# Optimization experiments

Measured on AMD Instinct MI355X. Metric: run time of the kernel, lower is better.

Reference implementation:

```python
import jax, jax.numpy as jnp
import numpy as np

E, T, H, I, K = 32, 2048, 1024, 512, 4


def setup_inputs() -> dict:
    key = jax.random.key(0)
    k1, k2, k3, k4, k5 = jax.random.split(key, 5)
    hidden_states = jax.random.normal(k1, (T, H), dtype=jnp.float32)
    top_k_index = jax.random.randint(k2, (T, K), 0, E)
    w = jax.random.uniform(k3, (T, K), dtype=jnp.float32)
    top_k_weights = w / jnp.sum(w, axis=-1, keepdims=True)  # router-like normalized weights
    gate_up_proj = jax.random.normal(k4, (E, 2 * I, H), dtype=jnp.float32) * 0.02
    down_proj = jax.random.normal(k5, (E, H, I), dtype=jnp.float32) * 0.02
    return {
        "hidden_states": hidden_states,
        "top_k_index": top_k_index,
        "top_k_weights": top_k_weights,
        "gate_up_proj": gate_up_proj,
        "down_proj": down_proj,
    }


def reference(hidden_states, top_k_index, top_k_weights, gate_up_proj, down_proj):
    # Faithful to the eager MoE dispatch loop: for each expert e, gather the
    # tokens routed to it, run gate/up/down SwiGLU, scale by routing weight,
    # and scatter-add into the output. Expressed as a scan over experts with a
    # per-token routing weight that is 0 for unrouted tokens (identical math:
    # index_add over (token, slot) pairs == sum_k where(idx==e, w, 0)).
    num_experts = gate_up_proj.shape[0]
    inter = down_proj.shape[2]

    def expert_step(acc, xs):
        gup_w, down_w, e = xs  # [2I, H], [H, I], scalar expert id
        # combined routing weight per token for this expert: [T]
        w_tok = jnp.sum(jnp.where(top_k_index == e, top_k_weights, 0.0), axis=1)
        gu = hidden_states @ gup_w.T              # [T, 2I]
        gate, up = gu[:, :inter], gu[:, inter:]
        h = jax.nn.silu(gate) * up                # [T, I]
        out = h @ down_w.T                        # [T, H]
        return acc + out * w_tok[:, None], None

    init = jnp.zeros_like(hidden_states)
    final_hidden_states, _ = jax.lax.scan(
        expert_step, init,
        (gate_up_proj, down_proj, jnp.arange(num_experts)),
    )
    return final_hidden_states
```

## Files before the change

kernel.cpp:

```cpp
#include <hip/hip_runtime.h>

#define NE 32
#define NT 2048
#define NH 1024
#define NI 512
#define NK 4
#define CAP 512

typedef __attribute__((ext_vector_type(8))) short short8;
typedef __attribute__((ext_vector_type(4))) float floatx4;

#define VMWAIT(n) asm volatile("s_waitcnt vmcnt(" #n ")" ::: "memory")
#define FBAR() do { __builtin_amdgcn_sched_barrier(0);              \
                    __builtin_amdgcn_s_barrier();                   \
                    __builtin_amdgcn_sched_barrier(0); } while (0)

static __device__ __forceinline__ void gload16(const void* g, void* l) {
    __builtin_amdgcn_global_load_lds(
        (const __attribute__((address_space(1))) unsigned int*)g,
        (__attribute__((address_space(3))) unsigned int*)l, 16, 0, 0);
}

static __device__ __forceinline__ unsigned pk_bf16(float x, float y) {
#if __has_builtin(__builtin_amdgcn_cvt_pk_bf16_f32)
    typedef __attribute__((ext_vector_type(2))) __bf16 bf16x2;
    union { bf16x2 v; unsigned u; } c;
    c.v = __builtin_amdgcn_cvt_pk_bf16_f32(x, y);
    return c.u;
#else
    union { float f; unsigned u; } a, b;
    a.f = x; b.f = y;
    unsigned ua = (a.u + 0x7fffu + ((a.u >> 16) & 1u)) >> 16;
    unsigned ub = (b.u + 0x7fffu + ((b.u >> 16) & 1u)) >> 16;
    return (ua & 0xffffu) | (ub << 16);
#endif
}

static __device__ __forceinline__ short8 pack8(const float* p) {
    union { unsigned u[4]; short8 s; } c;
    c.u[0] = pk_bf16(p[0], p[1]);
    c.u[1] = pk_bf16(p[2], p[3]);
    c.u[2] = pk_bf16(p[4], p[5]);
    c.u[3] = pk_bf16(p[6], p[7]);
    return c.s;
}

static __device__ __forceinline__ unsigned short bf16_1(float x) {
    return (unsigned short)(pk_bf16(x, 0.f) & 0xffffu);
}

__global__ void route_kernel(const int* __restrict__ idx,
                             const float* __restrict__ w,
                             int* __restrict__ counts,
                             int* __restrict__ tok,
                             float* __restrict__ wgt) {
    int tid = blockIdx.x * blockDim.x + threadIdx.x;
    if (tid >= NT * NK) return;
    int e = idx[tid];
    int pos = atomicAdd(&counts[e], 1);
    if (pos < CAP) {
        tok[e * CAP + pos] = tid;
        wgt[e * CAP + pos] = w[tid];
    }
}

__global__ void cvt_hidden(const float* __restrict__ hidden,
                           unsigned short* __restrict__ hb16) {
    size_t i = (size_t)(blockIdx.x * 256 + threadIdx.x) * 8;
    float tmp[8];
    *(floatx4*)tmp       = *(const floatx4*)(hidden + i);
    *(floatx4*)(tmp + 4) = *(const floatx4*)(hidden + i + 4);
    *(short8*)(hb16 + i) = pack8(tmp);
}

__global__ __launch_bounds__(256, 3) void gateup_mfma(
    const unsigned short* __restrict__ hb16,
    const float* __restrict__ gup,
    const int* __restrict__ counts,
    const int* __restrict__ tok,
    unsigned short* __restrict__ hbuf)
{
    int e = blockIdx.z;
    int cnt = counts[e];
    int m0 = blockIdx.y * 128;
    if (m0 >= cnt) return;
    int j0 = blockIdx.x * 64;

    __shared__ __align__(16) char smem[49152];
    __shared__ int tks[128];

    int tid = threadIdx.x;
    if (tid < 128) {
        int mi = m0 + tid;
        tks[tid] = tok[e * CAP + (mi < cnt ? mi : m0)];
    }
    __syncthreads();

    int lane = tid & 63, wave = tid >> 6;

    const unsigned short* aptr[2];
#pragma unroll
    for (int i = 0; i < 2; i++) {
        int ar = wave * 32 + i * 16 + (lane >> 2);
        aptr[i] = hb16 + (size_t)(tks[ar] >> 2) * NH + (lane & 3) * 8;
    }
    const float* gup_e = gup + (size_t)e * (2 * NI) * NH;
    const float* bptr[4];
#pragma unroll
    for (int i = 0; i < 4; i++) {
        int br = wave * 32 + i * 8 + (lane >> 3);
        int gc = (lane & 7) ^ (br & 7);
        int grow = (br < 64) ? (j0 + br) : (NI + j0 + (br - 64));
        bptr[i] = gup_e + (size_t)grow * NH + gc * 4;
    }

    char* const A0 = smem;
    char* const B0 = smem + 8192;
    char* const A1 = smem + 24576;
    char* const B1 = smem + 32768;

    int wm = wave >> 1;
    int wv = wave & 1;
    int lcol = lane & 15;
    int quad = lane >> 4;

    floatx4 acc[4][4];
#pragma unroll
    for (int a = 0; a < 4; a++)
#pragma unroll
        for (int b = 0; b < 4; b++) acc[a][b] = (floatx4){0.f, 0.f, 0.f, 0.f};

    auto stage = [&](char* dA, char* dB, int h) {
#pragma unroll
        for (int i = 0; i < 2; i++)
            gload16(aptr[i] + h, dA + wave * 2048 + i * 1024);
#pragma unroll
        for (int i = 0; i < 4; i++)
            gload16(bptr[i] + h, dB + wave * 4096 + i * 1024);
    };
    auto mfma_step = [&](const char* sA, const char* sB) {
        short8 af[4], bfr[4];
#pragma unroll
        for (int mt = 0; mt < 4; mt++) {
            int r = wm * 64 + mt * 16 + lcol;
            af[mt] = *(const short8*)(sA + r * 64 + quad * 16);
        }
#pragma unroll
        for (int nt = 0; nt < 4; nt++) {
            int r = wv * 64 + nt * 16 + lcol;
            const char* rb = sB + r * 128;
            float4 lo = *(const float4*)(rb + (((quad * 2)     ^ (r & 7)) * 16));
            float4 hi = *(const float4*)(rb + (((quad * 2 + 1) ^ (r & 7)) * 16));
            union { unsigned u[4]; short8 s; } c;
            c.u[0] = pk_bf16(lo.x, lo.y);
            c.u[1] = pk_bf16(lo.z, lo.w);
            c.u[2] = pk_bf16(hi.x, hi.y);
            c.u[3] = pk_bf16(hi.z, hi.w);
            bfr[nt] = c.s;
        }
#pragma unroll
        for (int mt = 0; mt < 4; mt++)
#pragma unroll
            for (int nt = 0; nt < 4; nt++)
                acc[mt][nt] = __builtin_amdgcn_mfma_f32_16x16x32_bf16(
                    af[mt], bfr[nt], acc[mt][nt], 0, 0, 0);
    };

    stage(A0, B0, 0);
    for (int kk = 0; kk < 32; kk += 2) {
        stage(A1, B1, (kk + 1) * 32);
        VMWAIT(6);
        FBAR();
        mfma_step(A0, B0);
        FBAR();
        if (kk + 2 < 32) { stage(A0, B0, (kk + 2) * 32); VMWAIT(6); }
        else             { VMWAIT(0); }
        FBAR();
        mfma_step(A1, B1);
        FBAR();
    }

    float (*upb)[64][68] = (float(*)[64][68])smem;
    if (wv == 1) {
#pragma unroll
        for (int mt = 0; mt < 4; mt++)
#pragma unroll
            for (int nt = 0; nt < 4; nt++)
#pragma unroll
                for (int i = 0; i < 4; i++)
                    upb[wm][mt * 16 + quad * 4 + i][nt * 16 + lcol] = acc[mt][nt][i];
    }
    __syncthreads();
    if (wv == 0) {
#pragma unroll
        for (int mt = 0; mt < 4; mt++) {
#pragma unroll
            for (int i = 0; i < 4; i++) {
                int lm = mt * 16 + quad * 4 + i;
                int m = wm * 64 + lm;
                if (m0 + m < cnt) {
                    unsigned short* hp = hbuf + (size_t)tks[m] * NI + j0;
#pragma unroll
                    for (int nt = 0; nt < 4; nt++) {
                        float g = acc[mt][nt][i];
                        float u = upb[wm][lm][nt * 16 + lcol];
                        float h = g / (1.f + __expf(-g)) * u;
                        hp[nt * 16 + lcol] = bf16_1(h);
                    }
                }
            }
        }
    }
}

template<bool ATOMIC>
__global__ __launch_bounds__(256, 3) void down_mfma(
    const unsigned short* __restrict__ hbuf,
    const float* __restrict__ dwn,
    const int* __restrict__ counts,
    const int* __restrict__ tok,
    const float* __restrict__ wgt,
    float* __restrict__ outp)
{
    int e = blockIdx.z;
    int cnt = counts[e];
    int m0 = blockIdx.y * 128;
    if (m0 >= cnt) return;
    int n0 = blockIdx.x * 128;

    __shared__ __align__(16) char smem[49152];
    __shared__ int tks[128];
    __shared__ float wls[128];

    int tid = threadIdx.x;
    if (tid < 128) {
        int mi = m0 + tid;
        int src = e * CAP + (mi < cnt ? mi : m0);
        tks[tid] = tok[src];
        wls[tid] = wgt[src];
    }
    __syncthreads();

    int lane = tid & 63, wave = tid >> 6;

    const unsigned short* aptr[2];
#pragma unroll
    for (int i = 0; i < 2; i++) {
        int ar = wave * 32 + i * 16 + (lane >> 2);
        aptr[i] = hbuf + (size_t)tks[ar] * NI + (lane & 3) * 8;
    }
    const float* dwn_e = dwn + (size_t)e * NH * NI;
    const float* bptr[4];
#pragma unroll
    for (int i = 0; i < 4; i++) {
        int br = wave * 32 + i * 8 + (lane >> 3);
        int gc = (lane & 7) ^ (br & 7);
        bptr[i] = dwn_e + (size_t)(n0 + br) * NI + gc * 4;
    }

    char* const A0 = smem;
    char* const B0 = smem + 8192;
    char* const A1 = smem + 24576;
    char* const B1 = smem + 32768;

    int wm = wave >> 1, wn = wave & 1;
    int lcol = lane & 15;
    int quad = lane >> 4;

    floatx4 acc[4][4];
#pragma unroll
    for (int a = 0; a < 4; a++)
#pragma unroll
        for (int b = 0; b < 4; b++) acc[a][b] = (floatx4){0.f, 0.f, 0.f, 0.f};

    auto stage = [&](char* dA, char* dB, int h) {
#pragma unroll
        for (int i = 0; i < 2; i++)
            gload16(aptr[i] + h, dA + wave * 2048 + i * 1024);
#pragma unroll
        for (int i = 0; i < 4; i++)
            gload16(bptr[i] + h, dB + wave * 4096 + i * 1024);
    };
    auto mfma_step = [&](const char* sA, const char* sB) {
        short8 af[4], bfr[4];
#pragma unroll
        for (int mt = 0; mt < 4; mt++) {
            int r = wm * 64 + mt * 16 + lcol;
            af[mt] = *(const short8*)(sA + r * 64 + quad * 16);
        }
#pragma unroll
        for (int nt = 0; nt < 4; nt++) {
            int r = wn * 64 + nt * 16 + lcol;
            const char* rb = sB + r * 128;
            float4 lo = *(const float4*)(rb + (((quad * 2)     ^ (r & 7)) * 16));
            float4 hi = *(const float4*)(rb + (((quad * 2 + 1) ^ (r & 7)) * 16));
            union { unsigned u[4]; short8 s; } c;
            c.u[0] = pk_bf16(lo.x, lo.y);
            c.u[1] = pk_bf16(lo.z, lo.w);
            c.u[2] = pk_bf16(hi.x, hi.y);
            c.u[3] = pk_bf16(hi.z, hi.w);
            bfr[nt] = c.s;
        }
#pragma unroll
        for (int mt = 0; mt < 4; mt++)
#pragma unroll
            for (int nt = 0; nt < 4; nt++)
                acc[mt][nt] = __builtin_amdgcn_mfma_f32_16x16x32_bf16(
                    af[mt], bfr[nt], acc[mt][nt], 0, 0, 0);
    };

    stage(A0, B0, 0);
    for (int kk = 0; kk < 16; kk += 2) {
        stage(A1, B1, (kk + 1) * 32);
        VMWAIT(6);
        FBAR();
        mfma_step(A0, B0);
        FBAR();
        if (kk + 2 < 16) { stage(A0, B0, (kk + 2) * 32); VMWAIT(6); }
        else             { VMWAIT(0); }
        FBAR();
        mfma_step(A1, B1);
        FBAR();
    }

#pragma unroll
    for (int mt = 0; mt < 4; mt++)
#pragma unroll
        for (int i = 0; i < 4; i++) {
            int m = wm * 64 + mt * 16 + quad * 4 + i;
            if (m0 + m < cnt) {
                float wl = wls[m];
                if (ATOMIC) {
                    float* op = outp + (size_t)(tks[m] >> 2) * NH + n0 + wn * 64;
#pragma unroll
                    for (int nt = 0; nt < 4; nt++)
                        atomicAdd(op + nt * 16 + lcol, acc[mt][nt][i] * wl);
                } else {
                    float* op = outp + (size_t)tks[m] * NH + n0 + wn * 64;
#pragma unroll
                    for (int nt = 0; nt < 4; nt++)
                        op[nt * 16 + lcol] = acc[mt][nt][i] * wl;
                }
            }
        }
}

__global__ void reduce_pairs(const float* __restrict__ pairbuf,
                             float* __restrict__ out) {
    int i = blockIdx.x * 256 + threadIdx.x;
    int t = i / (NH / 4);
    int c = (i - t * (NH / 4)) * 4;
    const float* p = pairbuf + (size_t)t * NK * NH + c;
    floatx4 a = *(const floatx4*)p;
    a += *(const floatx4*)(p + NH);
    a += *(const floatx4*)(p + 2 * NH);
    a += *(const floatx4*)(p + 3 * NH);
    *(floatx4*)(out + (size_t)t * NH + c) = a;
}

extern "C" void kernel_launch(void* const* d_in, const int* in_sizes, int n_in,
                              void* d_out, int out_size, void* d_ws, size_t ws_size,
                              hipStream_t stream) {
    const float* hidden = (const float*)d_in[0];
    const int*   tk_idx = (const int*)d_in[1];
    const float* tk_w   = (const float*)d_in[2];
    const float* gup    = (const float*)d_in[3];
    const float* dwn    = (const float*)d_in[4];
    float* out = (float*)d_out;

    char* ws = (char*)d_ws;
    int*            counts = (int*)ws;
    int*            tok    = (int*)(ws + 256);
    float*          wgt    = (float*)(ws + 256 + NE * CAP * 4);
    unsigned short* hb16   = (unsigned short*)(ws + 256 + 2 * NE * CAP * 4);
    unsigned short* hbuf   = (unsigned short*)(ws + 256 + 2 * NE * CAP * 4
                                               + (size_t)NT * NH * 2);
    float*          pairbuf = (float*)(ws + 256 + 2 * NE * CAP * 4
                                       + (size_t)NT * NH * 2
                                       + (size_t)NT * NK * NI * 2);

    size_t need = 256 + 2 * (size_t)NE * CAP * 4 + (size_t)NT * NH * 2
                + (size_t)NT * NK * NI * 2 + (size_t)NT * NK * NH * 4;
    bool pair_ok = ws_size >= need;

    hipMemsetAsync(counts, 0, 256, stream);

    route_kernel<<<(NT * NK + 255) / 256, 256, 0, stream>>>(tk_idx, tk_w, counts, tok, wgt);
    cvt_hidden<<<(NT * NH / 8) / 256, 256, 0, stream>>>(hidden, hb16);

    dim3 gridG(NI / 64, CAP / 128, NE);
    gateup_mfma<<<gridG, 256, 0, stream>>>(hb16, gup, counts, tok, hbuf);

    dim3 gridD(NH / 128, CAP / 128, NE);
    if (pair_ok) {
        down_mfma<false><<<gridD, 256, 0, stream>>>(hbuf, dwn, counts, tok, wgt, pairbuf);
        reduce_pairs<<<(NT * NH / 4) / 256, 256, 0, stream>>>(pairbuf, out);
    } else {
        hipMemsetAsync(out, 0, (size_t)NT * NH * sizeof(float), stream);
        down_mfma<true><<<gridD, 256, 0, stream>>>(hbuf, dwn, counts, tok, wgt, out);
    }
}
```

Before: 376.7 us.

## Rework MoE GEMM pipeline: bigger M tiles, register-staged bf16 B, triple-buffered A

Both expert GEMM kernels move to 512-thread blocks with 256-row token tiles and a 64-wide K step. The fp32 weight tile is now loaded into registers, converted to bf16 once and written to swizzled LDS. Previously every wave re-read fp32 weights from LDS and converted them before each MFMA. A tiles use a three-deep async global-to-LDS ring and B tiles a two-deep buffer, with explicit vmcnt/lgkmcnt barriers. The change cuts redundant conversion and LDS traffic and deepens overlap. In exchange it uses 128KB of LDS per block, which limits residency to one block per CU, and it launches fewer, coarser blocks, which may underfill the GPU given roughly 256 tokens per expert.

New measurement: 343.9 us. 1.1x faster.

```diff
diff --git a/kernel.cpp b/kernel.cpp
--- a/kernel.cpp
+++ b/kernel.cpp
@@ -11,9 +11,10 @@
 typedef __attribute__((ext_vector_type(4))) float floatx4;
 
 #define VMWAIT(n) asm volatile("s_waitcnt vmcnt(" #n ")" ::: "memory")
-#define FBAR() do { __builtin_amdgcn_sched_barrier(0);              \
-                    __builtin_amdgcn_s_barrier();                   \
-                    __builtin_amdgcn_sched_barrier(0); } while (0)
+#define LGKM_BAR() do { __builtin_amdgcn_sched_barrier(0);           \
+                        asm volatile("s_waitcnt lgkmcnt(0)" ::: "memory"); \
+                        __builtin_amdgcn_s_barrier();                \
+                        __builtin_amdgcn_sched_barrier(0); } while (0)
 
 static __device__ __forceinline__ void gload16(const void* g, void* l) {
     __builtin_amdgcn_global_load_lds(
@@ -73,56 +74,51 @@
     *(short8*)(hb16 + i) = pack8(tmp);
 }
 
-__global__ __launch_bounds__(256, 3) void gateup_mfma(
+__global__ __launch_bounds__(512, 2) void gateup_mfma(
     const unsigned short* __restrict__ hb16,
     const float* __restrict__ gup,
     const int* __restrict__ counts,
     const int* __restrict__ tok,
     unsigned short* __restrict__ hbuf)
 {
+    const int NTL = NH / 64;
     int e = blockIdx.z;
     int cnt = counts[e];
-    int m0 = blockIdx.y * 128;
+    int m0 = blockIdx.y * 256;
     if (m0 >= cnt) return;
     int j0 = blockIdx.x * 64;
 
-    __shared__ __align__(16) char smem[49152];
-    __shared__ int tks[128];
+    __shared__ __align__(16) char smem[131072];
+    __shared__ int tks[256];
 
     int tid = threadIdx.x;
-    if (tid < 128) {
+    if (tid < 256) {
         int mi = m0 + tid;
         tks[tid] = tok[e * CAP + (mi < cnt ? mi : m0)];
     }
     __syncthreads();
 
     int lane = tid & 63, wave = tid >> 6;
-
-    const unsigned short* aptr[2];
-#pragma unroll
-    for (int i = 0; i < 2; i++) {
-        int ar = wave * 32 + i * 16 + (lane >> 2);
-        aptr[i] = hb16 + (size_t)(tks[ar] >> 2) * NH + (lane & 3) * 8;
+    int wm = wave >> 1, wn = wave & 1;
+    int lcol = lane & 15, quad = lane >> 4;
+
+    const unsigned short* aptr[4];
+#pragma unroll
+    for (int i = 0; i < 4; i++) {
+        int r = wave * 32 + i * 8 + (lane >> 3);
+        int gc = (lane & 7) ^ (r & 7);
+        aptr[i] = hb16 + (size_t)(tks[r] >> 2) * NH + gc * 8;
     }
     const float* gup_e = gup + (size_t)e * (2 * NI) * NH;
-    const float* bptr[4];
+    int brow = wave * 16 + (lane >> 2);
+    int bgrow = (brow < 64) ? (j0 + brow) : (NI + j0 + (brow - 64));
+    const float* bsrc = gup_e + (size_t)bgrow * NH + (lane & 3) * 4;
+    int wboff[4];
 #pragma unroll
     for (int i = 0; i < 4; i++) {
-        int br = wave * 32 + i * 8 + (lane >> 3);
-        int gc = (lane & 7) ^ (br & 7);
-        int grow = (br < 64) ? (j0 + br) : (NI + j0 + (br - 64));
-        bptr[i] = gup_e + (size_t)grow * NH + gc * 4;
-    }
-
-    char* const A0 = smem;
-    char* const B0 = smem + 8192;
-    char* const A1 = smem + 24576;
-    char* const B1 = smem + 32768;
-
-    int wm = wave >> 1;
-    int wv = wave & 1;
-    int lcol = lane & 15;
-    int quad = lane >> 4;
+        int c16 = ((lane & 3) >> 1) + i * 2;
+        wboff[i] = brow * 128 + ((c16 ^ (brow & 7)) * 16) + (lane & 1) * 8;
+    }
 
     floatx4 acc[4][4];
 #pragma unroll
@@ -130,58 +126,74 @@
 #pragma unroll
         for (int b = 0; b < 4; b++) acc[a][b] = (floatx4){0.f, 0.f, 0.f, 0.f};
 
-    auto stage = [&](char* dA, char* dB, int h) {
-#pragma unroll
-        for (int i = 0; i < 2; i++)
-            gload16(aptr[i] + h, dA + wave * 2048 + i * 1024);
+    float4 rbE[4], rbO[4];
+
+    auto stageA = [&](int t) {
+        char* d = smem + (size_t)(t % 3) * 32768 + wave * 4096;
 #pragma unroll
         for (int i = 0; i < 4; i++)
-            gload16(bptr[i] + h, dB + wave * 4096 + i * 1024);
-    };
-    auto mfma_step = [&](const char* sA, const char* sB) {
-        short8 af[4], bfr[4];
-#pragma unroll
-        for (int mt = 0; mt < 4; mt++) {
-            int r = wm * 64 + mt * 16 + lcol;
-            af[mt] = *(const short8*)(sA + r * 64 + quad * 16);
-        }
-#pragma unroll
-        for (int nt = 0; nt < 4; nt++) {
-            int r = wv * 64 + nt * 16 + lcol;
-            const char* rb = sB + r * 128;
-            float4 lo = *(const float4*)(rb + (((quad * 2)     ^ (r & 7)) * 16));
-            float4 hi = *(const float4*)(rb + (((quad * 2 + 1) ^ (r & 7)) * 16));
-            union { unsigned u[4]; short8 s; } c;
-            c.u[0] = pk_bf16(lo.x, lo.y);
-            c.u[1] = pk_bf16(lo.z, lo.w);
-            c.u[2] = pk_bf16(hi.x, hi.y);
-            c.u[3] = pk_bf16(hi.z, hi.w);
-            bfr[nt] = c.s;
-        }
-#pragma unroll
-        for (int mt = 0; mt < 4; mt++)
-#pragma unroll
-            for (int nt = 0; nt < 4; nt++)
-                acc[mt][nt] = __builtin_amdgcn_mfma_f32_16x16x32_bf16(
-                    af[mt], bfr[nt], acc[mt][nt], 0, 0, 0);
-    };
-
-    stage(A0, B0, 0);
-    for (int kk = 0; kk < 32; kk += 2) {
-        stage(A1, B1, (kk + 1) * 32);
-        VMWAIT(6);
-        FBAR();
-        mfma_step(A0, B0);
-        FBAR();
-        if (kk + 2 < 32) { stage(A0, B0, (kk + 2) * 32); VMWAIT(6); }
-        else             { VMWAIT(0); }
-        FBAR();
-        mfma_step(A1, B1);
-        FBAR();
+            gload16(aptr[i] + t * 64, d + i * 1024);
+    };
+    auto loadB = [&](int t, float4* rb) {
+#pragma unroll
+        for (int i = 0; i < 4; i++)
+            rb[i] = *(const float4*)(bsrc + t * 64 + i * 16);
+    };
+    auto writeB = [&](int t, const float4* rb) {
+        char* d = smem + 98304 + (size_t)(t & 1) * 16384;
+#pragma unroll
+        for (int i = 0; i < 4; i++) {
+            uint2 u;
+            u.x = pk_bf16(rb[i].x, rb[i].y);
+            u.y = pk_bf16(rb[i].z, rb[i].w);
+            *(uint2*)(d + wboff[i]) = u;
+        }
+    };
+    auto mfma_t = [&](int t) {
+        const char* sA = smem + (size_t)(t % 3) * 32768;
+        const char* sB = smem + 98304 + (size_t)(t & 1) * 16384;
+#pragma unroll
+        for (int ks = 0; ks < 2; ks++) {
+            short8 af[4], bfr[4];
+#pragma unroll
+            for (int mt = 0; mt < 4; mt++) {
+                int r = wm * 64 + mt * 16 + lcol;
+                af[mt] = *(const short8*)(sA + r * 128 + ((((ks << 2) + quad) ^ (r & 7)) * 16));
+            }
+#pragma unroll
+            for (int nt = 0; nt < 4; nt++) {
+                int r = wn * 64 + nt * 16 + lcol;
+                bfr[nt] = *(const short8*)(sB + r * 128 + ((((ks << 2) + quad) ^ (r & 7)) * 16));
+            }
+#pragma unroll
+            for (int mt = 0; mt < 4; mt++)
+#pragma unroll
+                for (int nt = 0; nt < 4; nt++)
+                    acc[mt][nt] = __builtin_amdgcn_mfma_f32_16x16x32_bf16(
+                        af[mt], bfr[nt], acc[mt][nt], 0, 0, 0);
+        }
+    };
+    auto phase = [&](int t, float4* rbL, float4* rbW) {
+        if (t + 2 < NTL) { stageA(t + 2); loadB(t + 2, rbL); }
+        if (t + 1 < NTL) writeB(t + 1, rbW);
+        mfma_t(t);
+        if (t + 2 < NTL) { VMWAIT(8); } else { VMWAIT(0); }
+        LGKM_BAR();
+    };
+
+    stageA(0); loadB(0, rbE);
+    stageA(1); loadB(1, rbO);
+    writeB(0, rbE);
+    VMWAIT(8);
+    LGKM_BAR();
+
+    for (int tt = 0; tt < NTL; tt += 2) {
+        phase(tt,     rbE, rbO);
+        phase(tt + 1, rbO, rbE);
     }
 
     float (*upb)[64][68] = (float(*)[64][68])smem;
-    if (wv == 1) {
+    if (wn == 1) {
 #pragma unroll
         for (int mt = 0; mt < 4; mt++)
 #pragma unroll
@@ -191,7 +203,7 @@
                     upb[wm][mt * 16 + quad * 4 + i][nt * 16 + lcol] = acc[mt][nt][i];
     }
     __syncthreads();
-    if (wv == 0) {
+    if (wn == 0) {
 #pragma unroll
         for (int mt = 0; mt < 4; mt++) {
 #pragma unroll
@@ -214,7 +226,7 @@
 }
 
 template<bool ATOMIC>
-__global__ __launch_bounds__(256, 3) void down_mfma(
+__global__ __launch_bounds__(512, 2) void down_mfma(
     const unsigned short* __restrict__ hbuf,
     const float* __restrict__ dwn,
     const int* __restrict__ counts,
@@ -222,18 +234,19 @@
     const float* __restrict__ wgt,
     float* __restrict__ outp)
 {
+    const int NTL = NI / 64;
     int e = blockIdx.z;
     int cnt = counts[e];
-    int m0 = blockIdx.y * 128;
+    int m0 = blockIdx.y * 256;
     if (m0 >= cnt) return;
     int n0 = blockIdx.x * 128;
 
-    __shared__ __align__(16) char smem[49152];
-    __shared__ int tks[128];
-    __shared__ float wls[128];
+    __shared__ __align__(16) char smem[131072];
+    __shared__ int tks[256];
+    __shared__ float wls[256];
 
     int tid = threadIdx.x;
-    if (tid < 128) {
+    if (tid < 256) {
         int mi = m0 + tid;
         int src = e * CAP + (mi < cnt ? mi : m0);
         tks[tid] = tok[src];
@@ -242,30 +255,25 @@
     __syncthreads();
 
     int lane = tid & 63, wave = tid >> 6;
-
-    const unsigned short* aptr[2];
-#pragma unroll
-    for (int i = 0; i < 2; i++) {
-        int ar = wave * 32 + i * 16 + (lane >> 2);
-        aptr[i] = hbuf + (size_t)tks[ar] * NI + (lane & 3) * 8;
+    int wm = wave >> 1, wn = wave & 1;
+    int lcol = lane & 15, quad = lane >> 4;
+
+    const unsigned short* aptr[4];
+#pragma unroll
+    for (int i = 0; i < 4; i++) {
+        int r = wave * 32 + i * 8 + (lane >> 3);
+        int gc = (lane & 7) ^ (r & 7);
+        aptr[i] = hbuf + (size_t)tks[r] * NI + gc * 8;
     }
     const float* dwn_e = dwn + (size_t)e * NH * NI;
-    const float* bptr[4];
+    int brow = wave * 16 + (lane >> 2);
+    const float* bsrc = dwn_e + (size_t)(n0 + brow) * NI + (lane & 3) * 4;
+    int wboff[4];
 #pragma unroll
     for (int i = 0; i < 4; i++) {
-        int br = wave * 32 + i * 8 + (lane >> 3);
-        int gc = (lane & 7) ^ (br & 7);
-        bptr[i] = dwn_e + (size_t)(n0 + br) * NI + gc * 4;
-    }
-
-    char* const A0 = smem;
-    char* const B0 = smem + 8192;
-    char* const A1 = smem + 24576;
-    char* const B1 = smem + 32768;
-
-    int wm = wave >> 1, wn = wave & 1;
-    int lcol = lane & 15;
-    int quad = lane >> 4;
+        int c16 = ((lane & 3) >> 1) + i * 2;
+        wboff[i] = brow * 128 + ((c16 ^ (brow & 7)) * 16) + (lane & 1) * 8;
+    }
 
     floatx4 acc[4][4];
 #pragma unroll
@@ -273,54 +281,70 @@
 #pragma unroll
         for (int b = 0; b < 4; b++) acc[a][b] = (floatx4){0.f, 0.f, 0.f, 0.f};
 
-    auto stage = [&](char* dA, char* dB, int h) {
-#pragma unroll
-        for (int i = 0; i < 2; i++)
-            gload16(aptr[i] + h, dA + wave * 2048 + i * 1024);
+    float4 rbE[4], rbO[4];
+
+    auto stageA = [&](int t) {
+        char* d = smem + (size_t)(t % 3) * 32768 + wave * 4096;
 #pragma unroll
         for (int i = 0; i < 4; i++)
-            gload16(bptr[i] + h, dB + wave * 4096 + i * 1024);
-    };
-    auto mfma_step = [&](const char* sA, const char* sB) {
-        short8 af[4], bfr[4];
-#pragma unroll
-        for (int mt = 0; mt < 4; mt++) {
-            int r = wm * 64 + mt * 16 + lcol;
-            af[mt] = *(const short8*)(sA + r * 64 + quad * 16);
-        }
-#pragma unroll
-        for (int nt = 0; nt < 4; nt++) {
-            int r = wn * 64 + nt * 16 + lcol;
-            const char* rb = sB + r * 128;
-            float4 lo = *(const float4*)(rb + (((quad * 2)     ^ (r & 7)) * 16));
-            float4 hi = *(const float4*)(rb + (((quad * 2 + 1) ^ (r & 7)) * 16));
-            union { unsigned u[4]; short8 s; } c;
-            c.u[0] = pk_bf16(lo.x, lo.y);
-            c.u[1] = pk_bf16(lo.z, lo.w);
-            c.u[2] = pk_bf16(hi.x, hi.y);
-            c.u[3] = pk_bf16(hi.z, hi.w);
-            bfr[nt] = c.s;
-        }
-#pragma unroll
-        for (int mt = 0; mt < 4; mt++)
-#pragma unroll
-            for (int nt = 0; nt < 4; nt++)
-                acc[mt][nt] = __builtin_amdgcn_mfma_f32_16x16x32_bf16(
-                    af[mt], bfr[nt], acc[mt][nt], 0, 0, 0);
-    };
-
-    stage(A0, B0, 0);
-    for (int kk = 0; kk < 16; kk += 2) {
-        stage(A1, B1, (kk + 1) * 32);
-        VMWAIT(6);
-        FBAR();
-        mfma_step(A0, B0);
-        FBAR();
-        if (kk + 2 < 16) { stage(A0, B0, (kk + 2) * 32); VMWAIT(6); }
-        else             { VMWAIT(0); }
-        FBAR();
-        mfma_step(A1, B1);
-        FBAR();
+            gload16(aptr[i] + t * 64, d + i * 1024);
+    };
+    auto loadB = [&](int t, float4* rb) {
+#pragma unroll
+        for (int i = 0; i < 4; i++)
+            rb[i] = *(const float4*)(bsrc + t * 64 + i * 16);
+    };
+    auto writeB = [&](int t, const float4* rb) {
+        char* d = smem + 98304 + (size_t)(t & 1) * 16384;
+#pragma unroll
+        for (int i = 0; i < 4; i++) {
+            uint2 u;
+            u.x = pk_bf16(rb[i].x, rb[i].y);
+            u.y = pk_bf16(rb[i].z, rb[i].w);
+            *(uint2*)(d + wboff[i]) = u;
+        }
+    };
+    auto mfma_t = [&](int t) {
+        const char* sA = smem + (size_t)(t % 3) * 32768;
+        const char* sB = smem + 98304 + (size_t)(t & 1) * 16384;
+#pragma unroll
+        for (int ks = 0; ks < 2; ks++) {
+            short8 af[4], bfr[4];
+#pragma unroll
+            for (int mt = 0; mt < 4; mt++) {
+                int r = wm * 64 + mt * 16 + lcol;
+                af[mt] = *(const short8*)(sA + r * 128 + ((((ks << 2) + quad) ^ (r & 7)) * 16));
+            }
+#pragma unroll
+            for (int nt = 0; nt < 4; nt++) {
+                int r = wn * 64 + nt * 16 + lcol;
+                bfr[nt] = *(const short8*)(sB + r * 128 + ((((ks << 2) + quad) ^ (r & 7)) * 16));
+            }
+#pragma unroll
+            for (int mt = 0; mt < 4; mt++)
+#pragma unroll
+                for (int nt = 0; nt < 4; nt++)
+                    acc[mt][nt] = __builtin_amdgcn_mfma_f32_16x16x32_bf16(
+                        af[mt], bfr[nt], acc[mt][nt], 0, 0, 0);
+        }
+    };
+    auto phase = [&](int t, float4* rbL, float4* rbW) {
+        if (t + 2 < NTL) { stageA(t + 2); loadB(t + 2, rbL); }
+        if (t + 1 < NTL) writeB(t + 1, rbW);
+        mfma_t(t);
+        if (t + 2 < NTL) { VMWAIT(8); } else { VMWAIT(0); }
+        LGKM_BAR();
+    };
+
+    stageA(0); loadB(0, rbE);
+    stageA(1); loadB(1, rbO);
+    writeB(0, rbE);
+    VMWAIT(8);
+    LGKM_BAR();
+
+    for (int tt = 0; tt < NTL; tt += 2) {
+        phase(tt,     rbE, rbO);
+        phase(tt + 1, rbO, rbE);
     }
 
 #pragma unroll
@@ -388,15 +412,15 @@
     route_kernel<<<(NT * NK + 255) / 256, 256, 0, stream>>>(tk_idx, tk_w, counts, tok, wgt);
     cvt_hidden<<<(NT * NH / 8) / 256, 256, 0, stream>>>(hidden, hb16);
 
-    dim3 gridG(NI / 64, CAP / 128, NE);
-    gateup_mfma<<<gridG, 256, 0, stream>>>(hb16, gup, counts, tok, hbuf);
-
-    dim3 gridD(NH / 128, CAP / 128, NE);
+    dim3 gridG(NI / 64, CAP / 256, NE);
+    gateup_mfma<<<gridG, 512, 0, stream>>>(hb16, gup, counts, tok, hbuf);
+
+    dim3 gridD(NH / 128, CAP / 256, NE);
     if (pair_ok) {
-        down_mfma<false><<<gridD, 256, 0, stream>>>(hbuf, dwn, counts, tok, wgt, pairbuf);
+        down_mfma<false><<<gridD, 512, 0, stream>>>(hbuf, dwn, counts, tok, wgt, pairbuf);
         reduce_pairs<<<(NT * NH / 4) / 256, 256, 0, stream>>>(pairbuf, out);
     } else {
         hipMemsetAsync(out, 0, (size_t)NT * NH * sizeof(float), stream);
-        down_mfma<true><<<gridD, 256, 0, stream>>>(hbuf, dwn, counts, tok, wgt, out);
-    }
-}
+        down_mfma<true><<<gridD, 512, 0, stream>>>(hbuf, dwn, counts, tok, wgt, out);
+    }
+}
```
